# Performance work log

Hardware: AMD Instinct MI355X
Metric: run time of the kernel (lower is better)

Reference implementation:

```python
import jax, jax.numpy as jnp
import numpy as np

N_SIGMA = 1
K_INST = 8  # instance ids 1..K_INST (0 = background)
W_INST, W_VAR, W_SEED = 1.0, 10.0, 1.0
FG_WEIGHT = 1.0


def make_xym(h, w):
    # torch buffer: linspace(0,2,2048) x / linspace(0,1,1024) y, sliced to [0:h,0:w]
    xm = jnp.linspace(0.0, 2.0, 2048)[:w]
    ym = jnp.linspace(0.0, 1.0, 1024)[:h]
    return jnp.stack([jnp.broadcast_to(xm[None, :], (h, w)),
                      jnp.broadcast_to(ym[:, None], (h, w))], axis=0)  # [2,h,w]


def lovasz_hinge_flat(logits, labels):
    # logits, labels: [N] float (labels in {0,1})
    signs = 2.0 * labels - 1.0
    errors = 1.0 - logits * signs
    order = jnp.argsort(-errors)            # descending sort of errors
    errors_sorted = errors[order]
    gt_sorted = labels[order]
    gts = gt_sorted.sum()
    inter = gts - jnp.cumsum(gt_sorted)
    union = gts + jnp.cumsum(1.0 - gt_sorted)
    jac = 1.0 - inter / union
    grad = jnp.concatenate([jac[:1], jac[1:] - jac[:-1]])
    # torch impl wraps grad in Variable() -> no gradient through grad
    return jnp.dot(jax.nn.relu(errors_sorted), jax.lax.stop_gradient(grad))


def spatial_emb_loss(predictions, instances):
    B, C, T, h, w = predictions.shape
    xym = make_xym(h, w)
    # Faithful to the torch source: due to loop indentation, only the last
    # time step's var/instance/seed losses survive, and obj_count == 1.
    pred = predictions[:, :, T - 1]          # [B,C,h,w]
    inst = instances[:, 0, T - 1]            # [B,h,w] int
    spatial_emb = jnp.tanh(pred[:, 0:2]) + xym[None]   # [B,2,h,w]
    sigma = pred[:, 2:2 + N_SIGMA]                     # [B,1,h,w]
    seed = jax.nn.sigmoid(pred[:, 2 + N_SIGMA])        # [B,h,w]
    npix = float(h * w)

    def per_image(se, sig, sd, ins):
        bg_loss = jnp.sum(jnp.where(ins == 0, sd ** 2, 0.0))

        def per_id(k):
            m = (ins == k).astype(se.dtype)            # [h,w]
            cnt = m.sum()
            safe = jnp.maximum(cnt, 1.0)
            # to_center=True: center of in-mask pixel coordinates
            center = jnp.sum(xym * m[None], axis=(1, 2)) / safe      # [2]
            s_mean = jnp.sum(sig * m[None], axis=(1, 2)) / safe      # [n_sigma]
            var_l = jnp.sum(m[None] * (sig - jax.lax.stop_gradient(s_mean)[:, None, None]) ** 2) / (safe * N_SIGMA)
            s_exp = jnp.exp(s_mean * 10.0)
            dist = jnp.exp(-jnp.sum((se - center[:, None, None]) ** 2 * s_exp[:, None, None], axis=0))  # [h,w]
            inst_l = lovasz_hinge_flat((dist * 2.0 - 1.0).reshape(-1), m.reshape(-1))
            seed_l = FG_WEIGHT * jnp.sum(m * (sd - jax.lax.stop_gradient(dist)) ** 2)
            present = (cnt > 0).astype(se.dtype)       # torch skips absent ids
            return present * var_l, present * inst_l, present * seed_l

        var_l, inst_l, seed_l = jax.vmap(per_id)(jnp.arange(1, K_INST + 1))
        seed_loss = (bg_loss + seed_l.sum()) / npix
        # obj_count == 1 in the original code (incremented once per t-loop)
        return W_INST * inst_l.sum() + W_VAR * var_l.sum() + W_SEED * seed_loss

    per_b = jax.vmap(per_image)(spatial_emb, sigma, seed, inst)
    # torch: loss = loss / b, with b == B-1 after the loop
    return per_b.sum() / (B - 1)


def setup_inputs():
    key = jax.random.key(0)
    k1, k2 = jax.random.split(key)
    B, C, T, H, W = 4, 4, 2, 512, 1024
    predictions = jax.random.normal(k1, (B, C, T, H, W), dtype=jnp.float32)
    instances = jax.random.randint(k2, (B, 1, T, H, W), 0, K_INST + 1, dtype=jnp.int32)
    labels = jnp.zeros((B, 1, T, H, W), dtype=jnp.int32)  # unused by forward
    return {"predictions": predictions, "instances": instances, "labels": labels}


def reference(predictions, instances, labels):
    return spatial_emb_loss(predictions, instances)
```

## Files before the change

### kernel.cpp

```cpp
#include <hip/hip_runtime.h>

#define H 512
#define WID 1024
#define HW (H*WID)
#define B 4
#define K 8
#define NB 256
#define NBLK1 128

#define OFF_LOSS  0
#define OFF_CTRC  8
#define OFF_FIN   128
#define OFF_SPART 512
#define OFF_PART  21504

static __device__ __forceinline__ float frcp(float x){ return __builtin_amdgcn_rcpf(x); }
static __device__ __forceinline__ float fexp2(float x){ return __builtin_amdgcn_exp2f(x); }
static __device__ __forceinline__ float ftanh(float x){
  return 1.0f - 2.0f * frcp(__expf(2.0f*x) + 1.0f);
}
static __device__ __forceinline__ float fsigmoid(float x){
  return frcp(1.0f + __expf(-x));
}

__global__ __launch_bounds__(512) void k1_stats(const float* __restrict__ pred,
                                                const int* __restrict__ inst,
                                                float* __restrict__ ws) {
  const int b = blockIdx.y;
  __shared__ int4   ti[1024];
  __shared__ float4 ts[1024];
  __shared__ float  part5[K][5];
  const float4* sig4 = (const float4*)(pred + (size_t)(8*b + 5) * HW);
  const int4*   ins4 = (const int4*)(inst + (size_t)(2*b + 1) * HW);
  const int base4 = blockIdx.x * 1024;
  #pragma unroll
  for (int i = 0; i < 2; i++) {
    const int q = threadIdx.x + i*512;
    ti[q] = ins4[base4 + q];
    ts[q] = sig4[base4 + q];
  }
  __syncthreads();
  const int wv = threadIdx.x >> 6, lane = threadIdx.x & 63;
  const int kk = wv + 1;
  float cnt=0.f, sx=0.f, sy=0.f, ss=0.f, ss2=0.f;
  #pragma unroll
  for (int j = 0; j < 16; j++) {
    const int q = lane + 64*j;
    const int4   iv = ti[q];
    const float4 sv = ts[q];
    const int p = (base4 + q) * 4;
    const float xm0 = (float)(p & (WID-1)) * (2.0f/2047.0f);
    const float ym  = (float)(p >> 10)     * (1.0f/1023.0f);
    const float m0 = (iv.x==kk)?1.f:0.f, m1=(iv.y==kk)?1.f:0.f,
                m2 = (iv.z==kk)?1.f:0.f, m3=(iv.w==kk)?1.f:0.f;
    const float msum = (m0+m1)+(m2+m3);
    cnt += msum;
    sx  += msum*xm0 + (m1 + 2.0f*m2 + 3.0f*m3)*(2.0f/2047.0f);
    sy  += msum*ym;
    ss  += m0*sv.x + m1*sv.y + m2*sv.z + m3*sv.w;
    ss2 += m0*sv.x*sv.x + m1*sv.y*sv.y + m2*sv.z*sv.z + m3*sv.w*sv.w;
  }
  #pragma unroll
  for (int o=1;o<64;o<<=1){
    cnt+=__shfl_xor(cnt,o,64);
    sx +=__shfl_xor(sx, o,64);
    sy +=__shfl_xor(sy, o,64);
    ss +=__shfl_xor(ss, o,64);
    ss2+=__shfl_xor(ss2,o,64);
  }
  if (lane == 0) {
    part5[wv][0]=cnt; part5[wv][1]=sx; part5[wv][2]=sy; part5[wv][3]=ss; part5[wv][4]=ss2;
  }
  __syncthreads();
  if (threadIdx.x < K*5) {
    const int w = threadIdx.x / 5, c = threadIdx.x % 5;
    ws[OFF_SPART + ((size_t)(b*K + w)*NBLK1 + blockIdx.x)*5 + c] = part5[w][c];
  }
}

__global__ __launch_bounds__(256) void k2_fin(float* __restrict__ ws) {
  const int t = threadIdx.x;
  const int bk = t >> 3, s = t & 7;
  float a0=0.f,a1=0.f,a2=0.f,a3=0.f,a4=0.f;
  for (int j = 0; j < NBLK1/8; j++) {
    const float* p = ws + OFF_SPART + ((size_t)bk*NBLK1 + (s + 8*j))*5;
    a0+=p[0]; a1+=p[1]; a2+=p[2]; a3+=p[3]; a4+=p[4];
  }
  #pragma unroll
  for (int o=1;o<8;o<<=1){
    a0+=__shfl_xor(a0,o,64); a1+=__shfl_xor(a1,o,64); a2+=__shfl_xor(a2,o,64);
    a3+=__shfl_xor(a3,o,64); a4+=__shfl_xor(a4,o,64);
  }
  __shared__ float vloc[32];
  if (s == 0) {
    const float cnt=a0, sx=a1, sy=a2, ss=a3, ss2=a4;
    const float present = (cnt > 0.0f) ? 1.0f : 0.0f;
    const float safe = fmaxf(cnt, 1.0f);
    const float cx = sx/safe, cy = sy/safe, sm = ss/safe;
    const float var = (ss2 - 2.0f*sm*ss + sm*sm*cnt)/safe;
    const float sexp = expf(10.0f * sm);
    const float L2E = 1.4426950408889634f;
    float* fin = ws + OFF_FIN + bk*8;
    fin[0] = -sexp*L2E;
    fin[1] =  2.0f*sexp*cx*L2E;
    fin[2] =  2.0f*sexp*cy*L2E;
    fin[3] = -sexp*(cx*cx + cy*cy)*L2E + 8.0f;
    fin[4] = cnt;
    vloc[bk] = present * 10.0f * var * (1.0f/3.0f);
  }
  __syncthreads();
  if (t == 0) {
    float v = 0.f;
    #pragma unroll
    for (int i = 0; i < 32; i++) v += vloc[i];
    atomicAdd(ws + OFF_LOSS, v);
  }
}

template<int G>
__global__ __launch_bounds__(256) void k3_main(const float* __restrict__ pred,
                                               const int* __restrict__ inst,
                                               float* __restrict__ ws,
                                               unsigned int* __restrict__ part) {
  const int b = blockIdx.y, g = blockIdx.x;
  __shared__ unsigned int hist[K*NB];
  for (int i = threadIdx.x; i < K*NB; i += 256) hist[i] = 0;
  float4 fr[K];
  #pragma unroll
  for (int k=0;k<K;k++){
    const float* fin = ws + OFF_FIN + (b*K + k)*8;
    fr[k] = make_float4(fin[0], fin[1], fin[2], fin[3]);
  }
  __syncthreads();
  const float4* p0 = (const float4*)(pred + (size_t)(8*b+1)*HW);
  const float4* p1 = (const float4*)(pred + (size_t)(8*b+3)*HW);
  const float4* p3 = (const float4*)(pred + (size_t)(8*b+7)*HW);
  const int4*   in4 = (const int4*)(inst + (size_t)(2*b+1)*HW);
  float sAcc = 0.0f;
  constexpr int CH4 = HW / (G*4);
  const int base4 = g * CH4;
  #pragma unroll
  for (int q0 = 0; q0 < CH4; q0 += 256) {
    const int idx = base4 + q0 + threadIdx.x;
    const int4   iv = in4[idx];
    const float4 f0 = p0[idx];
    const float4 f1 = p1[idx];
    const float4 f3 = p3[idx];
    const int p = idx * 4;
    const float xm0 = (float)(p & (WID-1)) * (2.0f/2047.0f);
    const float ym  = (float)(p >> 10)     * (1.0f/1023.0f);
    const int   ivv[4] = {iv.x, iv.y, iv.z, iv.w};
    const float a0v[4] = {f0.x, f0.y, f0.z, f0.w};
    const float a1v[4] = {f1.x, f1.y, f1.z, f1.w};
    const float a3v[4] = {f3.x, f3.y, f3.z, f3.w};
    #pragma unroll
    for (int e4 = 0; e4 < 4; e4++) {
      const int ivp = ivv[e4];
      const float px = ftanh(a0v[e4]) + xm0 + (float)e4*(2.0f/2047.0f);
      const float py = ftanh(a1v[e4]) + ym;
      const float sd = fsigmoid(a3v[e4]);
      const float t2 = px*px + py*py;
      float down = 0.0f;
      #pragma unroll
      for (int j=0;j<K;j++){
        const float u = fmaf(fr[j].x, t2, fmaf(fr[j].y, px, fmaf(fr[j].z, py, fr[j].w)));
        const float v = fexp2(u);
        int vi = (int)v; vi = (vi > NB-1) ? NB-1 : vi;
        const bool own = (ivp == j+1);
        const int bu = own ? (NB-1 - vi) : vi;
        if (own) down = v;
        atomicAdd(&hist[j*NB + bu], own ? 0x10001u : 1u);
      }
      const float d  = (ivp == 0) ? 0.0f : down * (1.0f/256.0f);
      const float df = sd - d;
      sAcc += df*df;
    }
  }
  __syncthreads();
  unsigned int* dst = part + ((size_t)b*G + g)*(K*NB);
  for (int i = threadIdx.x; i < K*NB; i += 256) dst[i] = hist[i];
  #pragma unroll
  for (int o=1;o<64;o<<=1) sAcc += __shfl_xor(sAcc, o, 64);
  __shared__ float wsum[4];
  if ((threadIdx.x & 63) == 0) wsum[threadIdx.x>>6] = sAcc;
  __syncthreads();
  if (threadIdx.x == 0) {
    const float tot = wsum[0]+wsum[1]+wsum[2]+wsum[3];
    atomicAdd(ws + OFF_LOSS, tot * (1.0f/((float)HW * 3.0f)));
  }
}

__global__ __launch_bounds__(256) void kC_lovasz(const unsigned int* __restrict__ part,
                                                 float* __restrict__ ws,
                                                 float* __restrict__ out,
                                                 unsigned int* __restrict__ ctr, int G) {
  const int bk = blockIdx.x;
  const int b = bk >> 3, k = bk & 7;
  const int t = threadIdx.x, lane = t & 63, wv = t >> 6;
  const int bu = NB-1 - t;
  const unsigned int* base = part + (size_t)k*NB + bu;
  unsigned int rc = 0, rp = 0;
  #pragma unroll 8
  for (int g = 0; g < G; g++) {
    const unsigned int v = base[((size_t)b*G + g)*(K*NB)];
    rc += v & 0xFFFFu;
    rp += v >> 16;
  }
  const float cntF = ws[OFF_FIN + bk*8 + 4];
  int ic = (int)rc, ip = (int)rp;
  #pragma unroll
  for (int o=1;o<64;o<<=1){
    const int vc = __shfl_up(ic, o, 64);
    const int vp = __shfl_up(ip, o, 64);
    if (lane >= o) { ic += vc; ip += vp; }
  }
  __shared__ int wtc[4], wtp[4];
  if (lane == 63) { wtc[wv] = ic; wtp[wv] = ip; }
  __syncthreads();
  int offc = 0, offp = 0;
  for (int w = 0; w < wv; w++) { offc += wtc[w]; offp += wtp[w]; }
  int irun = offc + ic - (int)rc;
  int crun = offp + ip - (int)rp;
  double acc = 0.0;
  if (cntF > 0.0f && rc) {
    const double Pd = (double)cntF;
    const double jac0 = (irun==0) ? 0.0 : 1.0 - (Pd - crun)/(Pd + irun - crun);
    irun += (int)rc; crun += (int)rp;
    const double jac1 = 1.0 - (Pd - crun)/(Pd + irun - crun);
    acc = ((bu + 0.5) * (2.0/NB)) * (jac1 - jac0);
  }
  #pragma unroll
  for (int o=1;o<64;o<<=1) acc += __shfl_xor(acc, o, 64);
  __shared__ double racc[4];
  if (lane == 0) racc[wv] = acc;
  __syncthreads();
  if (t == 0) {
    const double tot = racc[0]+racc[1]+racc[2]+racc[3];
    atomicAdd(ws + OFF_LOSS, (float)(tot * (1.0/3.0)));
  }
  __threadfence();
  __shared__ int lastB;
  if (t == 0) lastB = (atomicAdd(ctr, 1u) == (unsigned)(B*K - 1)) ? 1 : 0;
  __syncthreads();
  if (lastB && t == 0) {
    __threadfence();
    out[0] = atomicAdd(ws + OFF_LOSS, 0.0f);
  }
}

extern "C" void kernel_launch(void* const* d_in, const int* in_sizes, int n_in,
                              void* d_out, int out_size, void* d_ws, size_t ws_size,
                              hipStream_t stream) {
  const float* pred = (const float*)d_in[0];
  const int*   inst = (const int*)d_in[1];
  float* ws  = (float*)d_ws;
  float* out = (float*)d_out;
  unsigned int* ctrC = ((unsigned int*)d_ws) + OFF_CTRC;
  unsigned int* part = ((unsigned int*)d_ws) + OFF_PART;
  int G = 256;
  if (ws_size < ((size_t)OFF_PART + (size_t)B*256*K*NB)*4) G = 128;
  hipMemsetAsync(d_ws, 0, 2048, stream);
  k1_stats<<<dim3(NBLK1,B), 512, 0, stream>>>(pred, inst, ws);
  k2_fin  <<<1, 256, 0, stream>>>(ws);
  if (G == 256) k3_main<256><<<dim3(256,B), 256, 0, stream>>>(pred, inst, ws, part);
  else          k3_main<128><<<dim3(128,B), 256, 0, stream>>>(pred, inst, ws, part);
  kC_lovasz<<<B*K, 256, 0, stream>>>(part, ws, out, ctrC, G);
}
```

Before: 146.5 us.

## Replace per-wave masked instance statistics with LDS atomic histogram accumulation

The stats kernel used to stage a tile in shared memory and have each of 8 waves scan the whole tile for one instance id. Now each pixel is read once, and its statistics are atomically added to shared-memory bins for its instance. Count, x-sum and y-sum are packed into a single 64-bit integer atomic, and sigma sums use float atomics. This removes the 8x redundant LDS scan and the shuffle reductions. The cost is heavy atomic contention on only 8 bins and non-deterministic float summation order.

```diff
diff --git a/kernel.cpp b/kernel.cpp
--- a/kernel.cpp
+++ b/kernel.cpp
@@ -23,58 +23,39 @@
   return frcp(1.0f + __expf(-x));
 }
 
-__global__ __launch_bounds__(512) void k1_stats(const float* __restrict__ pred,
+__global__ __launch_bounds__(256) void k1_stats(const float* __restrict__ pred,
                                                 const int* __restrict__ inst,
                                                 float* __restrict__ ws) {
   const int b = blockIdx.y;
-  __shared__ int4   ti[1024];
-  __shared__ float4 ts[1024];
-  __shared__ float  part5[K][5];
+  __shared__ unsigned long long tA[K];
+  __shared__ float tS[K], tS2[K];
+  if (threadIdx.x < K) { tA[threadIdx.x] = 0ull; tS[threadIdx.x] = 0.f; tS2[threadIdx.x] = 0.f; }
+  __syncthreads();
   const float4* sig4 = (const float4*)(pred + (size_t)(8*b + 5) * HW);
   const int4*   ins4 = (const int4*)(inst + (size_t)(2*b + 1) * HW);
   const int base4 = blockIdx.x * 1024;
   #pragma unroll
-  for (int i = 0; i < 2; i++) {
-    const int q = threadIdx.x + i*512;
-    ti[q] = ins4[base4 + q];
-    ts[q] = sig4[base4 + q];
-  }
-  __syncthreads();
-  const int wv = threadIdx.x >> 6, lane = threadIdx.x & 63;
-  const int kk = wv + 1;
-  float cnt=0.f, sx=0.f, sy=0.f, ss=0.f, ss2=0.f;
-  #pragma unroll
-  for (int j = 0; j < 16; j++) {
-    const int q = lane + 64*j;
-    const int4   iv = ti[q];
-    const float4 sv = ts[q];
-    const int p = (base4 + q) * 4;
-    const float xm0 = (float)(p & (WID-1)) * (2.0f/2047.0f);
-    const float ym  = (float)(p >> 10)     * (1.0f/1023.0f);
-    const float m0 = (iv.x==kk)?1.f:0.f, m1=(iv.y==kk)?1.f:0.f,
-                m2 = (iv.z==kk)?1.f:0.f, m3=(iv.w==kk)?1.f:0.f;
-    const float msum = (m0+m1)+(m2+m3);
-    cnt += msum;
-    sx  += msum*xm0 + (m1 + 2.0f*m2 + 3.0f*m3)*(2.0f/2047.0f);
-    sy  += msum*ym;
-    ss  += m0*sv.x + m1*sv.y + m2*sv.z + m3*sv.w;
-    ss2 += m0*sv.x*sv.x + m1*sv.y*sv.y + m2*sv.z*sv.z + m3*sv.w*sv.w;
-  }
-  #pragma unroll
-  for (int o=1;o<64;o<<=1){
-    cnt+=__shfl_xor(cnt,o,64);
-    sx +=__shfl_xor(sx, o,64);
-    sy +=__shfl_xor(sy, o,64);
-    ss +=__shfl_xor(ss, o,64);
-    ss2+=__shfl_xor(ss2,o,64);
-  }
-  if (lane == 0) {
-    part5[wv][0]=cnt; part5[wv][1]=sx; part5[wv][2]=sy; part5[wv][3]=ss; part5[wv][4]=ss2;
-  }
-  __syncthreads();
-  if (threadIdx.x < K*5) {
-    const int w = threadIdx.x / 5, c = threadIdx.x % 5;
-    ws[OFF_SPART + ((size_t)(b*K + w)*NBLK1 + blockIdx.x)*5 + c] = part5[w][c];
+  for (int g = 0; g < 4; g++) {
+    const int q = base4 + threadIdx.x + 256*g;
+    const int4   iv = ins4[q];
+    const float4 sv = sig4[q];
+    const int p = q * 4;
+    const unsigned long long Ab = (unsigned long long)(unsigned)(p & 1023)
+                                | ((unsigned long long)(unsigned)(p >> 10) << 23)
+                                | (1ULL << 45);
+    if (iv.x) { atomicAdd(&tA[iv.x-1], Ab+0); atomicAdd(&tS[iv.x-1], sv.x); atomicAdd(&tS2[iv.x-1], sv.x*sv.x); }
+    if (iv.y) { atomicAdd(&tA[iv.y-1], Ab+1); atomicAdd(&tS[iv.y-1], sv.y); atomicAdd(&tS2[iv.y-1], sv.y*sv.y); }
+    if (iv.z) { atomicAdd(&tA[iv.z-1], Ab+2); atomicAdd(&tS[iv.z-1], sv.z); atomicAdd(&tS2[iv.z-1], sv.z*sv.z); }
+    if (iv.w) { atomicAdd(&tA[iv.w-1], Ab+3); atomicAdd(&tS[iv.w-1], sv.w); atomicAdd(&tS2[iv.w-1], sv.w*sv.w); }
+  }
+  __syncthreads();
+  if (threadIdx.x < K) {
+    const unsigned long long A = tA[threadIdx.x];
+    const float cnt = (float)(unsigned)(A >> 45);
+    const float sx  = (float)(unsigned)(A & 0x7FFFFFull)        * (2.0f/2047.0f);
+    const float sy  = (float)(unsigned)((A >> 23) & 0x3FFFFFull) * (1.0f/1023.0f);
+    float* r = ws + OFF_SPART + ((size_t)(b*K + threadIdx.x)*NBLK1 + blockIdx.x)*5;
+    r[0]=cnt; r[1]=sx; r[2]=sy; r[3]=tS[threadIdx.x]; r[4]=tS2[threadIdx.x];
   }
 }
 
@@ -260,7 +241,7 @@
   int G = 256;
   if (ws_size < ((size_t)OFF_PART + (size_t)B*256*K*NB)*4) G = 128;
   hipMemsetAsync(d_ws, 0, 2048, stream);
-  k1_stats<<<dim3(NBLK1,B), 512, 0, stream>>>(pred, inst, ws);
+  k1_stats<<<dim3(NBLK1,B), 256, 0, stream>>>(pred, inst, ws);
   k2_fin  <<<1, 256, 0, stream>>>(ws);
   if (G == 256) k3_main<256><<<dim3(256,B), 256, 0, stream>>>(pred, inst, ws, part);
   else          k3_main<128><<<dim3(128,B), 256, 0, stream>>>(pred, inst, ws, part);
```

Result: slower. 158.2 us (+8.0%).
